# Optimization experiments

Measured on AMD Instinct MI355X. Metric: run time of the kernel, lower is better.

Reference implementation:

```python
import jax, jax.numpy as jnp
import numpy as np

D_MODEL, D_FF, RANK = 1024, 4096, 128
BATCH, SEQ = 4, 2048


def setup_inputs() -> dict:
    key = jax.random.key(0)
    ks = jax.random.split(key, 9)
    s = 0.02  # typical transformer init scale
    return {
        "x": jax.random.normal(ks[0], (BATCH, SEQ, D_MODEL), jnp.float32),
        "cfc_U": jax.random.normal(ks[1], (D_MODEL, RANK), jnp.float32) * s,
        "cfc_S": jax.random.uniform(ks[2], (RANK,), jnp.float32, 0.5, 1.5),
        "cfc_V": jax.random.normal(ks[3], (D_FF, RANK), jnp.float32) * s,
        "cfc_bias": jax.random.normal(ks[4], (D_FF,), jnp.float32) * s,
        "cproj_U": jax.random.normal(ks[5], (D_FF, RANK), jnp.float32) * s,
        "cproj_S": jax.random.uniform(ks[6], (RANK,), jnp.float32, 0.5, 1.5),
        "cproj_V": jax.random.normal(ks[7], (D_MODEL, RANK), jnp.float32) * s,
        "cproj_bias": jax.random.normal(ks[8], (D_MODEL,), jnp.float32) * s,
    }


def reference(x, cfc_U, cfc_S, cfc_V, cfc_bias, cproj_U, cproj_S, cproj_V, cproj_bias):
    # c_fc_weight = (U * S) @ V^T  -> [d_model, d_ff];  h = x @ c_fc_weight + b
    cfc_w = (cfc_U * cfc_S[None, :]) @ cfc_V.T            # [D_MODEL, D_FF]
    h = jnp.einsum('bsd,df->bsf', x, cfc_w) + cfc_bias    # [B, S, D_FF]
    h = jax.nn.gelu(h, approximate=False)                 # nn.GELU() = exact erf
    cproj_w = (cproj_U * cproj_S[None, :]) @ cproj_V.T    # [D_FF, D_MODEL]
    out = jnp.einsum('bsf,fd->bsd', h, cproj_w) + cproj_bias
    return out
```

## Files before the change

### kernel.cpp

```cpp
#include <hip/hip_runtime.h>
#include <math.h>

#define D_MODEL 1024
#define D_FF    4096
#define RANK    128
#define M_ROWS  8192

typedef _Float16 f16;
typedef _Float16 f16x8 __attribute__((ext_vector_type(8)));
typedef float    f32x4 __attribute__((ext_vector_type(4)));

#define MFMA16(a, b, c) __builtin_amdgcn_mfma_f32_16x16x32_f16((a), (b), (c), 0, 0, 0)

__device__ __forceinline__ f16x8 ld8(const f16* p) { return *(const f16x8*)p; }

__device__ __forceinline__ f16x8 cvt8(float4 a0, float4 a1) {
    f16x8 r = { (f16)a0.x, (f16)a0.y, (f16)a0.z, (f16)a0.w,
                (f16)a1.x, (f16)a1.y, (f16)a1.z, (f16)a1.w };
    return r;
}

__device__ __forceinline__ float gelu_exact(float v) {
    return 0.5f * v * (1.0f + erff(v * 0.70710678118654752440f));
}

__global__ __launch_bounds__(256) void k_prep(
    const float* __restrict__ cfcU, const float* __restrict__ cfcS,
    const float* __restrict__ cfcV, const float* __restrict__ pjU,
    const float* __restrict__ pjS,  const float* __restrict__ pjV,
    f16* __restrict__ w1T, f16* __restrict__ v1,
    f16* __restrict__ w2T, f16* __restrict__ v2)
{
    int i = blockIdx.x * 256 + threadIdx.x;
    if (i < 131072) {
        int r = i >> 10, d = i & 1023;
        w1T[i] = (f16)(cfcU[d * RANK + r] * cfcS[r]);
    } else if (i < 655360) {
        int j = i - 131072;
        v1[j] = (f16)cfcV[j];
    } else if (i < 1179648) {
        int j = i - 655360;
        int r = j >> 12, f = j & 4095;
        w2T[j] = (f16)(pjU[f * RANK + r] * pjS[r]);
    } else if (i < 1310720) {
        int j = i - 1179648;
        v2[j] = (f16)pjV[j];
    }
}

__global__ __launch_bounds__(512, 2) void k_t1(
    const float* __restrict__ x, const f16* __restrict__ w1T,
    f16* __restrict__ t1p)
{
    __shared__ __align__(16) f16 w1s[128 * 520];

    const int tid  = threadIdx.x;
    const int lane = tid & 63;
    const int wv   = tid >> 6;
    const int wm   = wv & 3, wn = wv >> 2;
    const int m0b  = blockIdx.x * 64;
    const int h    = blockIdx.y;
    const int c    = lane & 15, q = lane >> 4;

#define LOADX(dst, kc)                                                          \
    _Pragma("unroll") for (int kb = 0; kb < 4; ++kb) {                          \
        const float* px = &x[(size_t)(m0b + wm * 16 + c) * D_MODEL +            \
                             h * 512 + (kc) * 128 + kb * 32 + q * 8];           \
        dst[kb][0] = *(const float4*)px;                                        \
        dst[kb][1] = *(const float4*)(px + 4); }

#define COMPUTEKC(src, kc)                                                      \
    _Pragma("unroll") for (int kb = 0; kb < 4; ++kb) {                          \
        f16x8 af = cvt8(src[kb][0], src[kb][1]);                                \
        _Pragma("unroll") for (int nt = 0; nt < 4; ++nt) {                      \
            f16x8 bf = *(const f16x8*)                                          \
                &w1s[(wn * 64 + nt * 16 + c) * 520 + (kc) * 128 + kb * 32 + q * 8]; \
            acc[nt] = MFMA16(af, bf, acc[nt]); } }

    float4 xa[4][2], xb[4][2];
    LOADX(xa, 0)

#pragma unroll
    for (int i = 0; i < 16; ++i) {
        int id = i * 512 + tid;
        int rr = id >> 6, k8 = id & 63;
        *(f16x8*)&w1s[rr * 520 + k8 * 8] =
            ld8(w1T + (size_t)rr * D_MODEL + h * 512 + k8 * 8);
    }
    __syncthreads();

    f32x4 acc[4] = {};
    LOADX(xb, 1)
    COMPUTEKC(xa, 0)
    LOADX(xa, 2)
    COMPUTEKC(xb, 1)
    LOADX(xb, 3)
    COMPUTEKC(xa, 2)
    COMPUTEKC(xb, 3)

    f16* o = t1p + (size_t)h * (M_ROWS * RANK);
#pragma unroll
    for (int nt = 0; nt < 4; ++nt)
#pragma unroll
        for (int i2 = 0; i2 < 4; ++i2)
            o[(size_t)(m0b + wm * 16 + q * 4 + i2) * RANK + wn * 64 + nt * 16 + c] =
                (f16)acc[nt][i2];
#undef LOADX
#undef COMPUTEKC
}

#define RED_STORE(buf, acc)                                            \
    _Pragma("unroll") for (int rt = 0; rt < 8; ++rt)                   \
    _Pragma("unroll") for (int i2 = 0; i2 < 4; ++i2)                   \
        (buf)[(q * 4 + i2) * 132 + rt * 16 + c] = (acc)[rt][i2];
#define RED_ADD(buf, acc)                                              \
    _Pragma("unroll") for (int rt = 0; rt < 8; ++rt)                   \
    _Pragma("unroll") for (int i2 = 0; i2 < 4; ++i2)                   \
        (acc)[rt][i2] += (buf)[(q * 4 + i2) * 132 + rt * 16 + c];

__device__ __forceinline__ void load_tiles(
    const f16* __restrict__ v1, const f16* __restrict__ w2T,
    int tid, int fb, f16x8 nv[4], f16x8 nw[4])
{
#pragma unroll
    for (int i = 0; i < 4; ++i) {
        int id = i * 512 + tid;
        nv[i] = ld8(v1 + (size_t)(fb + (id >> 4)) * RANK + (id & 15) * 8);
    }
#pragma unroll
    for (int i = 0; i < 4; ++i) {
        int id = i * 512 + tid;
        nw[i] = ld8(w2T + (size_t)(id >> 4) * D_FF + fb + (id & 15) * 8);
    }
}

__device__ __forceinline__ void fused_step(
    const f16* __restrict__ v1, const f16* __restrict__ w2T,
    const float* __restrict__ bfc,
    f16* v1s, f16* w2s, f16* hs,
    const f16x8 a2[4], f32x4 c3[8],
    f16x8 cv[4], f16x8 cw[4], f16x8 nv[4], f16x8 nw[4],
    int tid, int s, int it, bool prefetch)
{
    const int lane = tid & 63;
    const int wv   = tid >> 6;
    const int wf   = wv >> 2;
    const int c    = lane & 15, q = lane >> 4;
    const int fbase = s * 2048 + it * 128;

    if (prefetch)
        load_tiles(v1, w2T, tid, fbase + 128, nv, nw);

    __syncthreads();
#pragma unroll
    for (int i = 0; i < 4; ++i) {
        int id = i * 512 + tid;
        *(f16x8*)&v1s[(id >> 4) * 136 + (id & 15) * 8] = cv[i];
    }
#pragma unroll
    for (int i = 0; i < 4; ++i) {
        int id = i * 512 + tid;
        *(f16x8*)&w2s[(id >> 4) * 136 + (id & 15) * 8] = cw[i];
    }
    __syncthreads();

    const int f0 = fbase + wf * 64;

    f32x4 c2[4] = {};
#pragma unroll
    for (int nt = 0; nt < 4; ++nt)
#pragma unroll
        for (int kb = 0; kb < 4; ++kb) {
            f16x8 bf = *(const f16x8*)
                &v1s[(wf * 64 + nt * 16 + c) * 136 + kb * 32 + q * 8];
            c2[nt] = MFMA16(a2[kb], bf, c2[nt]);
        }

#pragma unroll
    for (int nt = 0; nt < 4; ++nt) {
        float b = bfc[f0 + nt * 16 + c];
#pragma unroll
        for (int i2 = 0; i2 < 4; ++i2)
            hs[(wv * 16 + q * 4 + i2) * 72 + nt * 16 + c] =
                (f16)gelu_exact(c2[nt][i2] + b);
    }
    asm volatile("s_waitcnt lgkmcnt(0)" ::: "memory");

#pragma unroll
    for (int kb2 = 0; kb2 < 2; ++kb2) {
        f16x8 a3 = *(const f16x8*)&hs[(wv * 16 + c) * 72 + kb2 * 32 + q * 8];
#pragma unroll
        for (int rt = 0; rt < 8; ++rt) {
            f16x8 bf = *(const f16x8*)
                &w2s[(rt * 16 + c) * 136 + wf * 64 + kb2 * 32 + q * 8];
            c3[rt] = MFMA16(a3, bf, c3[rt]);
        }
    }
    asm volatile("s_waitcnt lgkmcnt(0)" ::: "memory");
}

__global__ __launch_bounds__(512, 2) void k_fused(
    const f16* __restrict__ t1p, const f16* __restrict__ v1,
    const float* __restrict__ bfc, const f16* __restrict__ w2T,
    f16* __restrict__ t2p)
{
    __shared__ __align__(16) char smem[88064];
    f16*  v1s = (f16*)smem;
    f16*  w2s = (f16*)(smem + 34816);
    f16*  hs  = (f16*)(smem + 69632);
    float* red = (float*)smem;

    const int tid  = threadIdx.x;
    const int lane = tid & 63;
    const int wv   = tid >> 6;
    const int wm   = wv & 3, wf = wv >> 2;
    const int c    = lane & 15, q = lane >> 4;

    const int bx  = blockIdx.x;
    const int s   = (bx & 7) >> 2;
    const int mb  = (bx >> 3) * 4 + (bx & 3);
    const int m0b = mb * 64;

    f16x8 a2[4];
#pragma unroll
    for (int kb = 0; kb < 4; ++kb) {
        const size_t off = (size_t)(m0b + wm * 16 + c) * RANK + kb * 32 + q * 8;
        f16x8 p0 = ld8(t1p + off);
        f16x8 p1 = ld8(t1p + (size_t)(M_ROWS * RANK) + off);
#pragma unroll
        for (int e = 0; e < 8; ++e)
            a2[kb][e] = (f16)((float)p0[e] + (float)p1[e]);
    }

    f16x8 pv[4], pw[4], qv[4], qw[4];
    load_tiles(v1, w2T, tid, s * 2048, pv, pw);

    f32x4 c3[8] = {};
#pragma unroll 1
    for (int it = 0; it < 16; it += 2) {
        fused_step(v1, w2T, bfc, v1s, w2s, hs, a2, c3,
                   pv, pw, qv, qw, tid, s, it, true);
        fused_step(v1, w2T, bfc, v1s, w2s, hs, a2, c3,
                   qv, qw, pv, pw, tid, s, it + 1, it + 2 < 16);
    }

    __syncthreads();
    if (wf == 1) { RED_STORE(&red[wm * 16 * 132], c3) }
    __syncthreads();
    if (wf == 0) {
        RED_ADD(&red[wm * 16 * 132], c3)
        f16* o = t2p + (size_t)s * (M_ROWS * RANK);
#pragma unroll
        for (int rt = 0; rt < 8; ++rt)
#pragma unroll
            for (int i2 = 0; i2 < 4; ++i2)
                o[(size_t)(m0b + wm * 16 + q * 4 + i2) * RANK + rt * 16 + c] =
                    (f16)c3[rt][i2];
    }
}

__global__ __launch_bounds__(256, 2) void k_out(
    const f16* __restrict__ t2p, const f16* __restrict__ v2,
    const float* __restrict__ bpj, float* __restrict__ out)
{
    __shared__ __align__(16) f16 v2s[256 * 136];

    const int tid  = threadIdx.x;
    const int lane = tid & 63;
    const int wv   = tid >> 6;
    const int wm   = wv & 1, wn = wv >> 1;
    const int m0b  = blockIdx.x * 32;
    const int n0b  = blockIdx.y * 256;
    const int c    = lane & 15, q = lane >> 4;

#pragma unroll
    for (int i8 = 0; i8 < 16; ++i8) {
        int id = i8 * 256 + tid;
        int nn = id >> 4, k8 = id & 15;
        *(f16x8*)&v2s[nn * 136 + k8 * 8] =
            ld8(v2 + (size_t)(n0b + nn) * RANK + k8 * 8);
    }

    f16x8 a[4];
#pragma unroll
    for (int kb = 0; kb < 4; ++kb) {
        const size_t off = (size_t)(m0b + wm * 16 + c) * RANK + kb * 32 + q * 8;
        f16x8 p0 = ld8(t2p + off);
        f16x8 p1 = ld8(t2p + (size_t)(M_ROWS * RANK) + off);
#pragma unroll
        for (int e = 0; e < 8; ++e)
            a[kb][e] = (f16)((float)p0[e] + (float)p1[e]);
    }
    __syncthreads();

    f32x4 acc[8] = {};
#pragma unroll
    for (int nt = 0; nt < 8; ++nt)
#pragma unroll
        for (int kb = 0; kb < 4; ++kb) {
            f16x8 bf = *(const f16x8*)
                &v2s[(wn * 128 + nt * 16 + c) * 136 + kb * 32 + q * 8];
            acc[nt] = MFMA16(a[kb], bf, acc[nt]);
        }

#pragma unroll
    for (int nt = 0; nt < 8; ++nt) {
        float b = bpj[n0b + wn * 128 + nt * 16 + c];
#pragma unroll
        for (int i2 = 0; i2 < 4; ++i2)
            out[(size_t)(m0b + wm * 16 + q * 4 + i2) * D_MODEL +
                n0b + wn * 128 + nt * 16 + c] = acc[nt][i2] + b;
    }
}

extern "C" void kernel_launch(void* const* d_in, const int* in_sizes, int n_in,
                              void* d_out, int out_size, void* d_ws, size_t ws_size,
                              hipStream_t stream) {
    const float* x    = (const float*)d_in[0];
    const float* cfcU = (const float*)d_in[1];
    const float* cfcS = (const float*)d_in[2];
    const float* cfcV = (const float*)d_in[3];
    const float* cfcB = (const float*)d_in[4];
    const float* pjU  = (const float*)d_in[5];
    const float* pjS  = (const float*)d_in[6];
    const float* pjV  = (const float*)d_in[7];
    const float* pjB  = (const float*)d_in[8];
    float* out = (float*)d_out;

    f16* wsf = (f16*)d_ws;
    f16* t1p = wsf;
    f16* t2p = wsf + 2097152;
    f16* w1T = wsf + 4194304;
    f16* v1  = w1T + 131072;
    f16* w2T = v1  + 524288;
    f16* v2  = w2T + 524288;

    k_prep <<<dim3(5120), 256, 0, stream>>>(cfcU, cfcS, cfcV, pjU, pjS, pjV,
                                            w1T, v1, w2T, v2);
    k_t1   <<<dim3(M_ROWS / 64, 2), 512, 0, stream>>>(x, w1T, t1p);
    k_fused<<<dim3(256), 512, 0, stream>>>(t1p, v1, cfcB, w2T, t2p);
    k_out  <<<dim3(M_ROWS / 32, D_MODEL / 256), 256, 0, stream>>>(t2p, v2, pjB, out);
}
```

Measured before the change: 177.6 us.

## Restructure fused kernel to per-wave d_ff slices with register-fed weights and tree reduction

The fused kernel now gives each block 32 rows and each wave a 512-wide d_ff slice. Weights v1 and w2T are loaded straight from global memory into registers with a double-buffered prefetch, which removes the shared-memory staging and the per-step block barriers. Partial results from the eight waves are combined with a tree reduction in shared memory, and a single unsplit t2 is written, so k_out no longer sums two partials. Exact erf GELU is replaced by an Abramowitz-Stegun polynomial using fast exp and rcp, which cuts transcendental cost at some accuracy risk. Each wave now reads more weight data from global memory or L2, and register pressure grows.

```diff
diff --git a/kernel.cpp b/kernel.cpp
--- a/kernel.cpp
+++ b/kernel.cpp
@@ -20,8 +20,18 @@
     return r;
 }
 
-__device__ __forceinline__ float gelu_exact(float v) {
-    return 0.5f * v * (1.0f + erff(v * 0.70710678118654752440f));
+__device__ __forceinline__ float gelu_fast(float v) {
+    float u  = v * 0.70710678118654752440f;
+    float au = fabsf(u);
+    float t  = __builtin_amdgcn_rcpf(__builtin_fmaf(0.3275911f, au, 1.0f));
+    float e  = __expf(-au * au);
+    float p  = __builtin_fmaf(1.061405429f, t, -1.453152027f);
+    p = __builtin_fmaf(p, t, 1.421413741f);
+    p = __builtin_fmaf(p, t, -0.284496736f);
+    p = __builtin_fmaf(p, t, 0.254829592f);
+    float er = __builtin_fmaf(-p * t, e, 1.0f);
+    er = copysignf(er, u);
+    return 0.5f * v * (1.0f + er);
 }
 
 __global__ __launch_bounds__(256) void k_prep(
@@ -109,158 +119,139 @@
 #undef COMPUTEKC
 }
 
-#define RED_STORE(buf, acc)                                            \
-    _Pragma("unroll") for (int rt = 0; rt < 8; ++rt)                   \
-    _Pragma("unroll") for (int i2 = 0; i2 < 4; ++i2)                   \
-        (buf)[(q * 4 + i2) * 132 + rt * 16 + c] = (acc)[rt][i2];
-#define RED_ADD(buf, acc)                                              \
-    _Pragma("unroll") for (int rt = 0; rt < 8; ++rt)                   \
-    _Pragma("unroll") for (int i2 = 0; i2 < 4; ++i2)                   \
-        (acc)[rt][i2] += (buf)[(q * 4 + i2) * 132 + rt * 16 + c];
-
-__device__ __forceinline__ void load_tiles(
-    const f16* __restrict__ v1, const f16* __restrict__ w2T,
-    int tid, int fb, f16x8 nv[4], f16x8 nw[4])
-{
-#pragma unroll
-    for (int i = 0; i < 4; ++i) {
-        int id = i * 512 + tid;
-        nv[i] = ld8(v1 + (size_t)(fb + (id >> 4)) * RANK + (id & 15) * 8);
-    }
-#pragma unroll
-    for (int i = 0; i < 4; ++i) {
-        int id = i * 512 + tid;
-        nw[i] = ld8(w2T + (size_t)(id >> 4) * D_FF + fb + (id & 15) * 8);
-    }
-}
-
-__device__ __forceinline__ void fused_step(
-    const f16* __restrict__ v1, const f16* __restrict__ w2T,
-    const float* __restrict__ bfc,
-    f16* v1s, f16* w2s, f16* hs,
-    const f16x8 a2[4], f32x4 c3[8],
-    f16x8 cv[4], f16x8 cw[4], f16x8 nv[4], f16x8 nw[4],
-    int tid, int s, int it, bool prefetch)
-{
-    const int lane = tid & 63;
-    const int wv   = tid >> 6;
-    const int wf   = wv >> 2;
-    const int c    = lane & 15, q = lane >> 4;
-    const int fbase = s * 2048 + it * 128;
-
-    if (prefetch)
-        load_tiles(v1, w2T, tid, fbase + 128, nv, nw);
-
-    __syncthreads();
-#pragma unroll
-    for (int i = 0; i < 4; ++i) {
-        int id = i * 512 + tid;
-        *(f16x8*)&v1s[(id >> 4) * 136 + (id & 15) * 8] = cv[i];
-    }
-#pragma unroll
-    for (int i = 0; i < 4; ++i) {
-        int id = i * 512 + tid;
-        *(f16x8*)&w2s[(id >> 4) * 136 + (id & 15) * 8] = cw[i];
-    }
-    __syncthreads();
-
-    const int f0 = fbase + wf * 64;
-
-    f32x4 c2[4] = {};
-#pragma unroll
-    for (int nt = 0; nt < 4; ++nt)
-#pragma unroll
-        for (int kb = 0; kb < 4; ++kb) {
-            f16x8 bf = *(const f16x8*)
-                &v1s[(wf * 64 + nt * 16 + c) * 136 + kb * 32 + q * 8];
-            c2[nt] = MFMA16(a2[kb], bf, c2[nt]);
-        }
-
-#pragma unroll
-    for (int nt = 0; nt < 4; ++nt) {
-        float b = bfc[f0 + nt * 16 + c];
-#pragma unroll
-        for (int i2 = 0; i2 < 4; ++i2)
-            hs[(wv * 16 + q * 4 + i2) * 72 + nt * 16 + c] =
-                (f16)gelu_exact(c2[nt][i2] + b);
-    }
-    asm volatile("s_waitcnt lgkmcnt(0)" ::: "memory");
-
-#pragma unroll
-    for (int kb2 = 0; kb2 < 2; ++kb2) {
-        f16x8 a3 = *(const f16x8*)&hs[(wv * 16 + c) * 72 + kb2 * 32 + q * 8];
-#pragma unroll
-        for (int rt = 0; rt < 8; ++rt) {
-            f16x8 bf = *(const f16x8*)
-                &w2s[(rt * 16 + c) * 136 + wf * 64 + kb2 * 32 + q * 8];
-            c3[rt] = MFMA16(a3, bf, c3[rt]);
-        }
-    }
-    asm volatile("s_waitcnt lgkmcnt(0)" ::: "memory");
-}
-
 __global__ __launch_bounds__(512, 2) void k_fused(
     const f16* __restrict__ t1p, const f16* __restrict__ v1,
     const float* __restrict__ bfc, const f16* __restrict__ w2T,
-    f16* __restrict__ t2p)
+    f16* __restrict__ t2)
 {
-    __shared__ __align__(16) char smem[88064];
-    f16*  v1s = (f16*)smem;
-    f16*  w2s = (f16*)(smem + 34816);
-    f16*  hs  = (f16*)(smem + 69632);
-    float* red = (float*)smem;
+    __shared__ __align__(16) char smem[67584];
 
     const int tid  = threadIdx.x;
     const int lane = tid & 63;
     const int wv   = tid >> 6;
-    const int wm   = wv & 3, wf = wv >> 2;
     const int c    = lane & 15, q = lane >> 4;
-
-    const int bx  = blockIdx.x;
-    const int s   = (bx & 7) >> 2;
-    const int mb  = (bx >> 3) * 4 + (bx & 3);
-    const int m0b = mb * 64;
-
-    f16x8 a2[4];
-#pragma unroll
-    for (int kb = 0; kb < 4; ++kb) {
-        const size_t off = (size_t)(m0b + wm * 16 + c) * RANK + kb * 32 + q * 8;
-        f16x8 p0 = ld8(t1p + off);
-        f16x8 p1 = ld8(t1p + (size_t)(M_ROWS * RANK) + off);
-#pragma unroll
-        for (int e = 0; e < 8; ++e)
-            a2[kb][e] = (f16)((float)p0[e] + (float)p1[e]);
-    }
-
-    f16x8 pv[4], pw[4], qv[4], qw[4];
-    load_tiles(v1, w2T, tid, s * 2048, pv, pw);
-
-    f32x4 c3[8] = {};
+    const int m0b  = blockIdx.x * 32;
+    const int f00  = wv * 512;
+
+    char* hsb = &smem[wv * 4096];
+
+    f16x8 a2[2][4];
+#pragma unroll
+    for (int wm2 = 0; wm2 < 2; ++wm2)
+#pragma unroll
+        for (int kb = 0; kb < 4; ++kb) {
+            const size_t off = (size_t)(m0b + wm2 * 16 + c) * RANK + kb * 32 + q * 8;
+            f16x8 p0 = ld8(t1p + off);
+            f16x8 p1 = ld8(t1p + (size_t)(M_ROWS * RANK) + off);
+#pragma unroll
+            for (int e = 0; e < 8; ++e)
+                a2[wm2][kb][e] = (f16)((float)p0[e] + (float)p1[e]);
+        }
+
+    f32x4 c3[2][8] = {};
+
+#define LOADBV(BV, ch)                                                          \
+    { const int ff = f00 + (ch) * 64;                                           \
+      _Pragma("unroll") for (int nt = 0; nt < 4; ++nt)                          \
+      _Pragma("unroll") for (int kb = 0; kb < 4; ++kb)                          \
+          BV[nt][kb] = ld8(v1 + (size_t)(ff + nt * 16 + c) * RANK + kb * 32 + q * 8); }
+
+#define CHUNK(BV, BN, ch, PF)                                                   \
+    { const int f0 = f00 + (ch) * 64;                                           \
+                    \
+      f32x4 c2[2][4] = {};                                                      \
+      _Pragma("unroll") for (int nt = 0; nt < 4; ++nt)                          \
+      _Pragma("unroll") for (int kb = 0; kb < 4; ++kb) {                        \
+          c2[0][nt] = MFMA16(a2[0][kb], BV[nt][kb], c2[0][nt]);                 \
+          c2[1][nt] = MFMA16(a2[1][kb], BV[nt][kb], c2[1][nt]);                 \
+      }                                                                         \
+      if (PF) LOADBV(BN, (ch) + 1)         \
+      float bb[4];                                                              \
+      _Pragma("unroll") for (int nt = 0; nt < 4; ++nt)                          \
+          bb[nt] = bfc[f0 + nt * 16 + c];                                       \
+                    \
+      _Pragma("unroll") for (int wm2 = 0; wm2 < 2; ++wm2)                       \
+      _Pragma("unroll") for (int nt = 0; nt < 4; ++nt)                          \
+      _Pragma("unroll") for (int i2 = 0; i2 < 4; ++i2) {                        \
+          int row = wm2 * 16 + q * 4 + i2;                                      \
+          int col = ((nt * 16 + c) * 2) ^ ((row & 7) << 4);                     \
+          *(f16*)(hsb + row * 128 + col) =                                      \
+              (f16)gelu_fast(c2[wm2][nt][i2] + bb[nt]);                         \
+      }                                                                         \
+      asm volatile("s_waitcnt lgkmcnt(0)" ::: "memory");    \
+                            \
+      _Pragma("unroll") for (int kb2 = 0; kb2 < 2; ++kb2) {                     \
+          f16x8 bw[8];                                                          \
+          _Pragma("unroll") for (int rt = 0; rt < 8; ++rt)                      \
+              bw[rt] = ld8(w2T + (size_t)(rt * 16 + c) * D_FF +                 \
+                           f0 + kb2 * 32 + q * 8);                              \
+          f16x8 a3[2];                                                          \
+          _Pragma("unroll") for (int wm2 = 0; wm2 < 2; ++wm2) {                 \
+              int row = wm2 * 16 + c;                                           \
+              int col = (kb2 * 64 + q * 16) ^ ((row & 7) << 4);                 \
+              a3[wm2] = *(const f16x8*)(hsb + row * 128 + col);                 \
+          }                                                                     \
+          _Pragma("unroll") for (int rt = 0; rt < 8; ++rt) {                    \
+              c3[0][rt] = MFMA16(a3[0], bw[rt], c3[0][rt]);                     \
+              c3[1][rt] = MFMA16(a3[1], bw[rt], c3[1][rt]);                     \
+          }                                                                     \
+      }                                                                         \
+      asm volatile("s_waitcnt lgkmcnt(0)" ::: "memory");         \
+    }
+
+    f16x8 bva[4][4], bvb[4][4];
+    LOADBV(bva, 0)
 #pragma unroll 1
-    for (int it = 0; it < 16; it += 2) {
-        fused_step(v1, w2T, bfc, v1s, w2s, hs, a2, c3,
-                   pv, pw, qv, qw, tid, s, it, true);
-        fused_step(v1, w2T, bfc, v1s, w2s, hs, a2, c3,
-                   qv, qw, pv, pw, tid, s, it + 1, it + 2 < 16);
-    }
-
-    __syncthreads();
-    if (wf == 1) { RED_STORE(&red[wm * 16 * 132], c3) }
-    __syncthreads();
-    if (wf == 0) {
-        RED_ADD(&red[wm * 16 * 132], c3)
-        f16* o = t2p + (size_t)s * (M_ROWS * RANK);
-#pragma unroll
-        for (int rt = 0; rt < 8; ++rt)
-#pragma unroll
-            for (int i2 = 0; i2 < 4; ++i2)
-                o[(size_t)(m0b + wm * 16 + q * 4 + i2) * RANK + rt * 16 + c] =
-                    (f16)c3[rt][i2];
+    for (int ch = 0; ch < 8; ch += 2) {
+        CHUNK(bva, bvb, ch, true)
+        CHUNK(bvb, bva, ch + 1, ch + 2 < 8)
+    }
+#undef LOADBV
+#undef CHUNK
+
+    float* rbuf = (float*)smem;
+
+#define ST_C3(w)                                                                \
+    { float* rb = rbuf + (w) * 4224;                                            \
+      _Pragma("unroll") for (int wm2 = 0; wm2 < 2; ++wm2)                       \
+      _Pragma("unroll") for (int rt = 0; rt < 8; ++rt)                          \
+      _Pragma("unroll") for (int i2 = 0; i2 < 4; ++i2)                          \
+          rb[(wm2 * 16 + q * 4 + i2) * 132 + rt * 16 + c] = c3[wm2][rt][i2]; }
+#define ADD_C3(w)                                                               \
+    { float* rb = rbuf + (w) * 4224;                                            \
+      _Pragma("unroll") for (int wm2 = 0; wm2 < 2; ++wm2)                       \
+      _Pragma("unroll") for (int rt = 0; rt < 8; ++rt)                          \
+      _Pragma("unroll") for (int i2 = 0; i2 < 4; ++i2)                          \
+          c3[wm2][rt][i2] += rb[(wm2 * 16 + q * 4 + i2) * 132 + rt * 16 + c]; }
+
+    __syncthreads();
+    if (wv >= 4) ST_C3(wv - 4)
+    __syncthreads();
+    if (wv < 4) ADD_C3(wv)
+    __syncthreads();
+    if (wv == 2 || wv == 3) ST_C3(wv - 2)
+    __syncthreads();
+    if (wv < 2) ADD_C3(wv)
+    __syncthreads();
+    if (wv == 1) ST_C3(0)
+    __syncthreads();
+    if (wv == 0) { ADD_C3(0) ST_C3(1) }
+    __syncthreads();
+#undef ST_C3
+#undef ADD_C3
+
+    {
+        const int mrow = tid >> 4;
+        const int r8   = (tid & 15) * 8;
+        const float* rb = rbuf + 4224 + mrow * 132 + r8;
+        float4 lo = *(const float4*)rb;
+        float4 hi = *(const float4*)(rb + 4);
+        *(f16x8*)&t2[(size_t)(m0b + mrow) * RANK + r8] = cvt8(lo, hi);
     }
 }
 
 __global__ __launch_bounds__(256, 2) void k_out(
-    const f16* __restrict__ t2p, const f16* __restrict__ v2,
+    const f16* __restrict__ t2, const f16* __restrict__ v2,
     const float* __restrict__ bpj, float* __restrict__ out)
 {
     __shared__ __align__(16) f16 v2s[256 * 136];
@@ -283,14 +274,8 @@
 
     f16x8 a[4];
 #pragma unroll
-    for (int kb = 0; kb < 4; ++kb) {
-        const size_t off = (size_t)(m0b + wm * 16 + c) * RANK + kb * 32 + q * 8;
-        f16x8 p0 = ld8(t2p + off);
-        f16x8 p1 = ld8(t2p + (size_t)(M_ROWS * RANK) + off);
-#pragma unroll
-        for (int e = 0; e < 8; ++e)
-            a[kb][e] = (f16)((float)p0[e] + (float)p1[e]);
-    }
+    for (int kb = 0; kb < 4; ++kb)
+        a[kb] = ld8(t2 + (size_t)(m0b + wm * 16 + c) * RANK + kb * 32 + q * 8);
     __syncthreads();
 
     f32x4 acc[8] = {};
@@ -329,7 +314,7 @@
 
     f16* wsf = (f16*)d_ws;
     f16* t1p = wsf;
-    f16* t2p = wsf + 2097152;
+    f16* t2  = wsf + 2097152;
     f16* w1T = wsf + 4194304;
     f16* v1  = w1T + 131072;
     f16* w2T = v1  + 524288;
@@ -338,6 +323,6 @@
     k_prep <<<dim3(5120), 256, 0, stream>>>(cfcU, cfcS, cfcV, pjU, pjS, pjV,
                                             w1T, v1, w2T, v2);
     k_t1   <<<dim3(M_ROWS / 64, 2), 512, 0, stream>>>(x, w1T, t1p);
-    k_fused<<<dim3(256), 512, 0, stream>>>(t1p, v1, cfcB, w2T, t2p);
-    k_out  <<<dim3(M_ROWS / 32, D_MODEL / 256), 256, 0, stream>>>(t2p, v2, pjB, out);
-}
+    k_fused<<<dim3(M_ROWS / 32), 512, 0, stream>>>(t1p, v1, cfcB, w2T, t2);
+    k_out  <<<dim3(M_ROWS / 32, D_MODEL / 256), 256, 0, stream>>>(t2, v2, pjB, out);
+}
```

New measurement: 235.0 us. 32.3% more time.
